# Optimization experiments

Measured on AMD Instinct MI355X. Metric: run time of the kernel, lower is better.

## Reference

```python
import jax, jax.numpy as jnp
import numpy as np

NUM_CLASSES = 1000
EMB_DIM = 768
BATCH = 16384
EPS = 1e-8  # torch F.cosine_similarity eps


def setup_inputs() -> dict:
    key = jax.random.key(0)
    k1, k2, k3, k4 = jax.random.split(key, 4)
    embeddings = jax.random.normal(k1, (BATCH, EMB_DIM), dtype=jnp.float32)
    logits = jax.random.normal(k2, (BATCH, NUM_CLASSES), dtype=jnp.float32)
    targets = jax.random.randint(k3, (BATCH,), 0, NUM_CLASSES, dtype=jnp.int64 if jax.config.jax_enable_x64 else jnp.int32)
    centroids = jax.random.normal(k4, (NUM_CLASSES, EMB_DIM), dtype=jnp.float32)
    u = jnp.ones((1,), dtype=jnp.float32)
    return {"embeddings": embeddings, "logits": logits, "targets": targets,
            "centroids": centroids, "u": u}


def _cosine_sim(embeddings, centroids):
    # torch cosine_similarity: x / max(||x||, eps); formulated as normalize + GEMM
    en = embeddings / jnp.maximum(jnp.linalg.norm(embeddings, axis=1, keepdims=True), EPS)
    cn = centroids / jnp.maximum(jnp.linalg.norm(centroids, axis=1, keepdims=True), EPS)
    return jnp.einsum('nd,cd->nc', en, cn)  # [N, C]


def reference(embeddings, logits, targets, centroids, u):
    n_classes = centroids.shape[0]
    # cross entropy (mean reduction)
    logp = jax.nn.log_softmax(logits, axis=1)
    ce_loss = -jnp.mean(jnp.take_along_axis(logp, targets[:, None], axis=1))

    sim = _cosine_sim(embeddings, centroids)            # [N, C]
    soft_labels = jax.nn.softmax(sim, axis=1)           # [N, C]

    hard_one_hot = jax.nn.one_hot(targets, n_classes, dtype=jnp.float32)
    similarity_to_target = jnp.sum(soft_labels * hard_one_hot, axis=1)  # [N]
    discount = 1.0 - similarity_to_target
    reg_term = jnp.mean(discount) * u                   # shape (1,)

    # mse_loss(hard_one_hot, soft_labels.detach()) -- soft_labels detached
    dist_reg = jnp.mean((hard_one_hot - jax.lax.stop_gradient(soft_labels)) ** 2)

    return ce_loss + dist_reg + reg_term                # shape (1,)
```

## Files before the change

kernel.cpp:

```cpp
#include <hip/hip_runtime.h>
#include <hip/hip_bf16.h>
#include <stdint.h>

#define BATCH 16384
#define NCLS 1000
#define NPAD 1024
#define EMB 768
#define KT 12
#define BM 256
#define BN 256
#define ABYTES 16384
#define BUFB 32768
#define GEMM_BLKS 256

typedef __attribute__((ext_vector_type(4))) float f32x4;
typedef long v2i64 __attribute__((ext_vector_type(2)));

#define GLOAD16(g, l) __builtin_amdgcn_global_load_lds(              \
    (const __attribute__((address_space(1))) unsigned int*)(g),       \
    (__attribute__((address_space(3))) unsigned int*)(l), 16, 0, 0)

__global__ __launch_bounds__(256) void prep_ce(
    const float* __restrict__ emb, const float* __restrict__ cent,
    const float* __restrict__ logits, const int* __restrict__ targets,
    unsigned int* __restrict__ en8, unsigned int* __restrict__ cn8,
    float* __restrict__ ce_row)
{
    const int b    = blockIdx.x;
    const int lane = threadIdx.x & 63;
    const int warp = threadIdx.x >> 6;

    if (b >= 4352) {
        const int row = (b - 4352) * 4 + warp;
        const float* rp = logits + (size_t)row * NCLS;
        const float4* r4 = (const float4*)rp;
        float4 v0 = r4[lane];
        float4 v1 = r4[lane + 64];
        float4 v2 = r4[lane + 128];
        const bool has = lane < 58;
        float4 v3 = has ? r4[lane + 192] : v0;
        float s = __expf(v0.x) + __expf(v0.y) + __expf(v0.z) + __expf(v0.w)
                + __expf(v1.x) + __expf(v1.y) + __expf(v1.z) + __expf(v1.w)
                + __expf(v2.x) + __expf(v2.y) + __expf(v2.z) + __expf(v2.w);
        if (has) s += __expf(v3.x) + __expf(v3.y) + __expf(v3.z) + __expf(v3.w);
        #pragma unroll
        for (int m = 1; m < 64; m <<= 1) s += __shfl_xor(s, m, 64);
        if (lane == 0) {
            float xt = rp[targets[row]];
            ce_row[row] = __logf(s) - xt;
        }
        return;
    }

    const float* in; unsigned int* outp; int row, nvalid;
    if (b < 4096) { row = b * 4 + warp;          in = emb;  outp = en8; nvalid = BATCH; }
    else          { row = (b - 4096) * 4 + warp; in = cent; outp = cn8; nvalid = NCLS; }

    float vals[12] = {0,0,0,0,0,0,0,0,0,0,0,0};
    float ss = 0.f;
    if (row < nvalid) {
        const float4* rp = (const float4*)(in + (size_t)row * EMB);
        #pragma unroll
        for (int i = 0; i < 3; ++i) {
            float4 v = rp[lane + 64 * i];
            vals[4*i+0] = v.x; vals[4*i+1] = v.y; vals[4*i+2] = v.z; vals[4*i+3] = v.w;
            ss += v.x*v.x + v.y*v.y + v.z*v.z + v.w*v.w;
        }
    }
    #pragma unroll
    for (int m = 1; m < 64; m <<= 1) ss += __shfl_xor(ss, m, 64);
    float scale = (row < nvalid) ? (1.0f / fmaxf(sqrtf(ss), 1e-8f)) : 0.0f;

    unsigned int* op = outp + (size_t)row * (EMB / 4);
    #pragma unroll
    for (int i = 0; i < 3; ++i) {
        int p = 0;
        p = __builtin_amdgcn_cvt_pk_fp8_f32(vals[4*i+0] * scale, vals[4*i+1] * scale, p, false);
        p = __builtin_amdgcn_cvt_pk_fp8_f32(vals[4*i+2] * scale, vals[4*i+3] * scale, p, true);
        op[lane + 64 * i] = (unsigned int)p;
    }
}

__global__ __launch_bounds__(256, 1) void gemm_kernel(
    const uint8_t* __restrict__ en8, const uint8_t* __restrict__ cn8,
    const int* __restrict__ targets,
    float* __restrict__ partZ, float* __restrict__ partS2,
    float* __restrict__ et_out)
{
    __shared__ __align__(128) uint8_t lds[2][BUFB];

    const int bid  = blockIdx.x;
    const int tid  = threadIdx.x;
    const int lane = tid & 63;
    const int warp = tid >> 6;

    const int g   = bid & 7;
    const int s   = bid >> 3;
    const int mb  = g * 8 + (s >> 2);
    const int nb  = s & 3;
    const int R0  = mb * BM;
    const int Nc0 = nb * BN;
    const int wr  = warp >> 1;
    const int wc  = warp & 1;
    const int l15 = lane & 15;
    const int rq  = lane >> 4;

    const int csw  = ((tid & 3) * 16) ^ (((tid >> 3) & 3) << 4);
    const int srow = tid >> 2;
    size_t asrc[4], bsrc[4];
    #pragma unroll
    for (int j = 0; j < 4; ++j) {
        asrc[j] = (size_t)(R0  + j * 64 + srow) * EMB + csw;
        bsrc[j] = (size_t)(Nc0 + j * 64 + srow) * EMB + csw;
    }
    const uint8_t* enb = en8;
    const uint8_t* cnb = cn8;

#define STAGE(b, kt) do { const size_t ko = (size_t)(kt) * 64;               \
    _Pragma("unroll") for (int j = 0; j < 4; ++j)                            \
        GLOAD16(enb + asrc[j] + ko, &lds[b][j * 4096 + tid * 16]);           \
    _Pragma("unroll") for (int j = 0; j < 4; ++j)                            \
        GLOAD16(cnb + bsrc[j] + ko, &lds[b][ABYTES + j * 4096 + tid * 16]);  \
} while (0)

    const int cx   = (rq * 16) ^ (((l15 >> 1) & 3) << 4);
    const int aoff = (wr * 128 + l15) * 64 + cx;
    const int boff = ABYTES + (wc * 128 + l15) * 64 + cx;

    f32x4 acc[8][8];
    #pragma unroll
    for (int m = 0; m < 8; ++m)
        #pragma unroll
        for (int n = 0; n < 8; ++n) acc[m][n] = (f32x4){0.f, 0.f, 0.f, 0.f};

    STAGE(0, 0);
    __syncthreads();

    for (int kt = 0; kt < KT; ++kt) {
        const int buf = kt & 1;
        if (kt + 1 < KT) STAGE(buf ^ 1, kt + 1);
        const uint8_t* L = &lds[buf][0];
        v2i64 af[8], bf[8];
        #pragma unroll
        for (int m = 0; m < 8; ++m) af[m] = *(const v2i64*)(L + aoff + m * 1024);
        #pragma unroll
        for (int n = 0; n < 8; ++n) bf[n] = *(const v2i64*)(L + boff + n * 1024);
        #pragma unroll
        for (int kk = 0; kk < 2; ++kk)
            #pragma unroll
            for (int m = 0; m < 8; ++m)
                #pragma unroll
                for (int n = 0; n < 8; ++n)
                    acc[m][n] = __builtin_amdgcn_mfma_f32_16x16x32_fp8_fp8(
                        bf[n][kk], af[m][kk], acc[m][n], 0, 0, 0);
        __syncthreads();
    }
#undef STAGE

    const int plane = nb * 2 + wc;
    #pragma unroll
    for (int m = 0; m < 8; ++m) {
        const int row = R0 + wr * 128 + m * 16 + l15;
        const int t   = targets[row];
        float z = 0.f, s2 = 0.f;
        #pragma unroll
        for (int n = 0; n < 8; ++n) {
            const int cb = Nc0 + wc * 128 + n * 16 + rq * 4;
            #pragma unroll
            for (int r = 0; r < 4; ++r) {
                const bool valid = (cb + r) < NCLS;
                float e = valid ? __expf(acc[m][n][r]) : 0.f;
                z += e; s2 += e * e;
                if (cb + r == t) et_out[row] = e;
            }
        }
        z  += __shfl_xor(z, 16, 64);  z  += __shfl_xor(z, 32, 64);
        s2 += __shfl_xor(s2, 16, 64); s2 += __shfl_xor(s2, 32, 64);
        if (rq == 0) {
            partZ [(size_t)plane * BATCH + row] = z;
            partS2[(size_t)plane * BATCH + row] = s2;
        }
    }
}

__global__ __launch_bounds__(256) void finalize_kernel(
    const float* __restrict__ partZ, const float* __restrict__ partS2,
    const float* __restrict__ et_out, const float* __restrict__ ce_row,
    const float* __restrict__ u, float* __restrict__ out)
{
    __shared__ float red[4];
    const int row  = blockIdx.x * 256 + threadIdx.x;
    const int lane = threadIdx.x & 63;
    float z = 0.f, s2 = 0.f;
    #pragma unroll
    for (int i = 0; i < 8; ++i) {
        z  += partZ [(size_t)i * BATCH + row];
        s2 += partS2[(size_t)i * BATCH + row];
    }
    float et = et_out[row];
    float invz = 1.0f / z;
    float pt = et * invz;
    float c = (s2 * invz * invz - 2.0f * pt + 1.0f) * (1.0f / ((float)BATCH * (float)NCLS))
            + (1.0f - pt) * u[0] * (1.0f / (float)BATCH)
            + ce_row[row] * (1.0f / (float)BATCH);
    #pragma unroll
    for (int m = 1; m < 64; m <<= 1) c += __shfl_xor(c, m, 64);
    if (lane == 0) red[threadIdx.x >> 6] = c;
    __syncthreads();
    if (threadIdx.x == 0) atomicAdd(out, red[0] + red[1] + red[2] + red[3]);
}

extern "C" void kernel_launch(void* const* d_in, const int* in_sizes, int n_in,
                              void* d_out, int out_size, void* d_ws, size_t ws_size,
                              hipStream_t stream) {
    const float* emb       = (const float*)d_in[0];
    const float* logits    = (const float*)d_in[1];
    const int*   targets   = (const int*)d_in[2];
    const float* centroids = (const float*)d_in[3];
    const float* u         = (const float*)d_in[4];
    float* out = (float*)d_out;

    uint8_t* en8  = (uint8_t*)d_ws;
    uint8_t* cn8  = en8 + (size_t)BATCH * EMB;
    float* partZ  = (float*)(cn8 + (size_t)NPAD * EMB);
    float* partS2 = partZ + 8 * BATCH;
    float* et_out = partS2 + 8 * BATCH;
    float* ce_row = et_out + BATCH;

    hipMemsetAsync(d_out, 0, sizeof(float), stream);
    prep_ce<<<8448, 256, 0, stream>>>(emb, centroids, logits, targets,
                                      (unsigned int*)en8, (unsigned int*)cn8, ce_row);
    gemm_kernel<<<GEMM_BLKS, 256, 0, stream>>>(en8, cn8, targets, partZ, partS2, et_out);
    finalize_kernel<<<BATCH / 256, 256, 0, stream>>>(partZ, partS2, et_out, ce_row, u, out);
}
```

Measured before the change: 59.74 us.

## Fuse embedding and logits prep per wave, halve GEMM M-tile for more blocks

```diff
diff --git a/kernel.cpp b/kernel.cpp
--- a/kernel.cpp
+++ b/kernel.cpp
@@ -7,11 +7,13 @@
 #define NPAD 1024
 #define EMB 768
 #define KT 12
-#define BM 256
+#define BM 128
 #define BN 256
-#define ABYTES 16384
-#define BUFB 32768
-#define GEMM_BLKS 256
+#define ABYTES 8192
+#define BUFB 24576
+#define GEMM_BLKS 512
+#define PREP_MAIN 2048
+#define PREP_CENT 128
 
 typedef __attribute__((ext_vector_type(4))) float f32x4;
 typedef long v2i64 __attribute__((ext_vector_type(2)));
@@ -19,6 +21,19 @@
 #define GLOAD16(g, l) __builtin_amdgcn_global_load_lds(              \
     (const __attribute__((address_space(1))) unsigned int*)(g),       \
     (__attribute__((address_space(3))) unsigned int*)(l), 16, 0, 0)
+
+__device__ __forceinline__ float d4(float4 v) {
+    return v.x*v.x + v.y*v.y + v.z*v.z + v.w*v.w;
+}
+__device__ __forceinline__ float e4(float4 v) {
+    return __expf(v.x) + __expf(v.y) + __expf(v.z) + __expf(v.w);
+}
+__device__ __forceinline__ unsigned int pk8(float4 v, float s) {
+    int p = 0;
+    p = __builtin_amdgcn_cvt_pk_fp8_f32(v.x * s, v.y * s, p, false);
+    p = __builtin_amdgcn_cvt_pk_fp8_f32(v.z * s, v.w * s, p, true);
+    return (unsigned int)p;
+}
 
 __global__ __launch_bounds__(256) void prep_ce(
     const float* __restrict__ emb, const float* __restrict__ cent,
@@ -28,60 +43,74 @@
 {
     const int b    = blockIdx.x;
     const int lane = threadIdx.x & 63;
-    const int warp = threadIdx.x >> 6;
-
-    if (b >= 4352) {
-        const int row = (b - 4352) * 4 + warp;
-        const float* rp = logits + (size_t)row * NCLS;
-        const float4* r4 = (const float4*)rp;
-        float4 v0 = r4[lane];
-        float4 v1 = r4[lane + 64];
-        float4 v2 = r4[lane + 128];
+    const int w    = threadIdx.x >> 6;
+
+    if (b < PREP_MAIN) {
+        const int e0 = b * 8 + w * 2;
+        const float4* a0 = (const float4*)(emb + (size_t)e0 * EMB);
+        const float4* a1 = (const float4*)(emb + (size_t)(e0 + 1) * EMB);
+        const float4* r0 = (const float4*)(logits + (size_t)e0 * NCLS);
+        const float4* r1 = (const float4*)(logits + (size_t)(e0 + 1) * NCLS);
+
+        float4 ea0 = a0[lane], ea1 = a0[lane + 64], ea2 = a0[lane + 128];
+        float4 eb0 = a1[lane], eb1 = a1[lane + 64], eb2 = a1[lane + 128];
+        float4 la0 = r0[lane], la1 = r0[lane + 64], la2 = r0[lane + 128];
+        float4 lb0 = r1[lane], lb1 = r1[lane + 64], lb2 = r1[lane + 128];
         const bool has = lane < 58;
-        float4 v3 = has ? r4[lane + 192] : v0;
-        float s = __expf(v0.x) + __expf(v0.y) + __expf(v0.z) + __expf(v0.w)
-                + __expf(v1.x) + __expf(v1.y) + __expf(v1.z) + __expf(v1.w)
-                + __expf(v2.x) + __expf(v2.y) + __expf(v2.z) + __expf(v2.w);
-        if (has) s += __expf(v3.x) + __expf(v3.y) + __expf(v3.z) + __expf(v3.w);
-        #pragma unroll
-        for (int m = 1; m < 64; m <<= 1) s += __shfl_xor(s, m, 64);
+        float4 la3 = has ? r0[lane + 192] : la0;
+        float4 lb3 = has ? r1[lane + 192] : lb0;
+        const int t0 = targets[e0], t1 = targets[e0 + 1];
+        const float xt0 = logits[(size_t)e0 * NCLS + t0];
+        const float xt1 = logits[(size_t)(e0 + 1) * NCLS + t1];
+
+        float ss0 = d4(ea0) + d4(ea1) + d4(ea2);
+        float ss1 = d4(eb0) + d4(eb1) + d4(eb2);
+        #pragma unroll
+        for (int m = 1; m < 64; m <<= 1) {
+            ss0 += __shfl_xor(ss0, m, 64);
+            ss1 += __shfl_xor(ss1, m, 64);
+        }
+        const float sc0 = 1.0f / fmaxf(sqrtf(ss0), 1e-8f);
+        const float sc1 = 1.0f / fmaxf(sqrtf(ss1), 1e-8f);
+        unsigned int* o0 = en8 + (size_t)e0 * (EMB / 4);
+        unsigned int* o1 = o0 + (EMB / 4);
+        o0[lane] = pk8(ea0, sc0); o0[lane + 64] = pk8(ea1, sc0); o0[lane + 128] = pk8(ea2, sc0);
+        o1[lane] = pk8(eb0, sc1); o1[lane + 64] = pk8(eb1, sc1); o1[lane + 128] = pk8(eb2, sc1);
+
+        float s0 = e4(la0) + e4(la1) + e4(la2);
+        float s1 = e4(lb0) + e4(lb1) + e4(lb2);
+        if (has) { s0 += e4(la3); s1 += e4(lb3); }
+        #pragma unroll
+        for (int m = 1; m < 64; m <<= 1) {
+            s0 += __shfl_xor(s0, m, 64);
+            s1 += __shfl_xor(s1, m, 64);
+        }
         if (lane == 0) {
-            float xt = rp[targets[row]];
-            ce_row[row] = __logf(s) - xt;
+            ce_row[e0]     = __logf(s0) - xt0;
+            ce_row[e0 + 1] = __logf(s1) - xt1;
         }
         return;
     }
 
-    const float* in; unsigned int* outp; int row, nvalid;
-    if (b < 4096) { row = b * 4 + warp;          in = emb;  outp = en8; nvalid = BATCH; }
-    else          { row = (b - 4096) * 4 + warp; in = cent; outp = cn8; nvalid = NCLS; }
-
-    float vals[12] = {0,0,0,0,0,0,0,0,0,0,0,0};
-    float ss = 0.f;
-    if (row < nvalid) {
-        const float4* rp = (const float4*)(in + (size_t)row * EMB);
-        #pragma unroll
-        for (int i = 0; i < 3; ++i) {
-            float4 v = rp[lane + 64 * i];
-            vals[4*i+0] = v.x; vals[4*i+1] = v.y; vals[4*i+2] = v.z; vals[4*i+3] = v.w;
-            ss += v.x*v.x + v.y*v.y + v.z*v.z + v.w*v.w;
-        }
-    }
-    #pragma unroll
-    for (int m = 1; m < 64; m <<= 1) ss += __shfl_xor(ss, m, 64);
-    float scale = (row < nvalid) ? (1.0f / fmaxf(sqrtf(ss), 1e-8f)) : 0.0f;
-
-    unsigned int* op = outp + (size_t)row * (EMB / 4);
-    #pragma unroll
-    for (int i = 0; i < 3; ++i) {
-        int p = 0;
-        p = __builtin_amdgcn_cvt_pk_fp8_f32(vals[4*i+0] * scale, vals[4*i+1] * scale, p, false);
-        p = __builtin_amdgcn_cvt_pk_fp8_f32(vals[4*i+2] * scale, vals[4*i+3] * scale, p, true);
-        op[lane + 64 * i] = (unsigned int)p;
-    }
-}
-
-__global__ __launch_bounds__(256, 1) void gemm_kernel(
+    const int c0 = (b - PREP_MAIN) * 8 + w * 2;
+    #pragma unroll
+    for (int p = 0; p < 2; ++p) {
+        const int row = c0 + p;
+        float4 v0 = {0,0,0,0}, v1 = {0,0,0,0}, v2 = {0,0,0,0};
+        if (row < NCLS) {
+            const float4* rp = (const float4*)(cent + (size_t)row * EMB);
+            v0 = rp[lane]; v1 = rp[lane + 64]; v2 = rp[lane + 128];
+        }
+        float ss = d4(v0) + d4(v1) + d4(v2);
+        #pragma unroll
+        for (int m = 1; m < 64; m <<= 1) ss += __shfl_xor(ss, m, 64);
+        const float sc = (row < NCLS) ? (1.0f / fmaxf(sqrtf(ss), 1e-8f)) : 0.0f;
+        unsigned int* op = cn8 + (size_t)row * (EMB / 4);
+        op[lane] = pk8(v0, sc); op[lane + 64] = pk8(v1, sc); op[lane + 128] = pk8(v2, sc);
+    }
+}
+
+__global__ __launch_bounds__(256, 2) void gemm_kernel(
     const uint8_t* __restrict__ en8, const uint8_t* __restrict__ cn8,
     const int* __restrict__ targets,
     float* __restrict__ partZ, float* __restrict__ partS2,
@@ -96,7 +125,7 @@
 
     const int g   = bid & 7;
     const int s   = bid >> 3;
-    const int mb  = g * 8 + (s >> 2);
+    const int mb  = g * 16 + (s >> 2);
     const int nb  = s & 3;
     const int R0  = mb * BM;
     const int Nc0 = nb * BN;
@@ -107,29 +136,28 @@
 
     const int csw  = ((tid & 3) * 16) ^ (((tid >> 3) & 3) << 4);
     const int srow = tid >> 2;
-    size_t asrc[4], bsrc[4];
-    #pragma unroll
-    for (int j = 0; j < 4; ++j) {
-        asrc[j] = (size_t)(R0  + j * 64 + srow) * EMB + csw;
-        bsrc[j] = (size_t)(Nc0 + j * 64 + srow) * EMB + csw;
-    }
+    size_t asrc[2], bsrc[4];
+    #pragma unroll
+    for (int j = 0; j < 2; ++j) asrc[j] = (size_t)(R0  + j * 64 + srow) * EMB + csw;
+    #pragma unroll
+    for (int j = 0; j < 4; ++j) bsrc[j] = (size_t)(Nc0 + j * 64 + srow) * EMB + csw;
     const uint8_t* enb = en8;
     const uint8_t* cnb = cn8;
 
 #define STAGE(b, kt) do { const size_t ko = (size_t)(kt) * 64;               \
-    _Pragma("unroll") for (int j = 0; j < 4; ++j)                            \
+    _Pragma("unroll") for (int j = 0; j < 2; ++j)                            \
         GLOAD16(enb + asrc[j] + ko, &lds[b][j * 4096 + tid * 16]);           \
     _Pragma("unroll") for (int j = 0; j < 4; ++j)                            \
         GLOAD16(cnb + bsrc[j] + ko, &lds[b][ABYTES + j * 4096 + tid * 16]);  \
 } while (0)
 
     const int cx   = (rq * 16) ^ (((l15 >> 1) & 3) << 4);
-    const int aoff = (wr * 128 + l15) * 64 + cx;
+    const int aoff = (wr * 64 + l15) * 64 + cx;
     const int boff = ABYTES + (wc * 128 + l15) * 64 + cx;
 
-    f32x4 acc[8][8];
-    #pragma unroll
-    for (int m = 0; m < 8; ++m)
+    f32x4 acc[4][8];
+    #pragma unroll
+    for (int m = 0; m < 4; ++m)
         #pragma unroll
         for (int n = 0; n < 8; ++n) acc[m][n] = (f32x4){0.f, 0.f, 0.f, 0.f};
 
@@ -140,15 +168,15 @@
         const int buf = kt & 1;
         if (kt + 1 < KT) STAGE(buf ^ 1, kt + 1);
         const uint8_t* L = &lds[buf][0];
-        v2i64 af[8], bf[8];
-        #pragma unroll
-        for (int m = 0; m < 8; ++m) af[m] = *(const v2i64*)(L + aoff + m * 1024);
+        v2i64 af[4], bf[8];
+        #pragma unroll
+        for (int m = 0; m < 4; ++m) af[m] = *(const v2i64*)(L + aoff + m * 1024);
         #pragma unroll
         for (int n = 0; n < 8; ++n) bf[n] = *(const v2i64*)(L + boff + n * 1024);
         #pragma unroll
         for (int kk = 0; kk < 2; ++kk)
             #pragma unroll
-            for (int m = 0; m < 8; ++m)
+            for (int m = 0; m < 4; ++m)
                 #pragma unroll
                 for (int n = 0; n < 8; ++n)
                     acc[m][n] = __builtin_amdgcn_mfma_f32_16x16x32_fp8_fp8(
@@ -159,8 +187,8 @@
 
     const int plane = nb * 2 + wc;
     #pragma unroll
-    for (int m = 0; m < 8; ++m) {
-        const int row = R0 + wr * 128 + m * 16 + l15;
+    for (int m = 0; m < 4; ++m) {
+        const int row = R0 + wr * 64 + m * 16 + l15;
         const int t   = targets[row];
         float z = 0.f, s2 = 0.f;
         #pragma unroll
@@ -228,8 +256,8 @@
     float* ce_row = et_out + BATCH;
 
     hipMemsetAsync(d_out, 0, sizeof(float), stream);
-    prep_ce<<<8448, 256, 0, stream>>>(emb, centroids, logits, targets,
-                                      (unsigned int*)en8, (unsigned int*)cn8, ce_row);
+    prep_ce<<<PREP_MAIN + PREP_CENT, 256, 0, stream>>>(emb, centroids, logits, targets,
+                                                       (unsigned int*)en8, (unsigned int*)cn8, ce_row);
     gemm_kernel<<<GEMM_BLKS, 256, 0, stream>>>(en8, cn8, targets, partZ, partS2, et_out);
     finalize_kernel<<<BATCH / 256, 256, 0, stream>>>(partZ, partS2, et_out, ce_row, u, out);
 }
```

Result: faster. 54.76 us (-8.3%).
